# Kernel optimization log

Measured on AMD Instinct MI355X. Metric: run time of the kernel, lower is better.

The kernel has to match this reference:

```python
import jax, jax.numpy as jnp
import numpy as np

DIM = 512
NUM_GROUPS = 32
EPS = 1e-6
INV_SQRT2 = 0.7071067811865476


def group_norm(x, gamma, beta):
    # x: [b, c, h, w]; GroupNorm with NUM_GROUPS groups, per-channel affine
    b, c, h, w = x.shape
    xg = x.reshape(b, NUM_GROUPS, c // NUM_GROUPS, h, w)
    mu = xg.mean(axis=(2, 3, 4), keepdims=True)
    var = xg.var(axis=(2, 3, 4), keepdims=True)
    xn = ((xg - mu) * jax.lax.rsqrt(var + EPS)).reshape(b, c, h, w)
    return xn * gamma[None, :, None, None] + beta[None, :, None, None]


def conv1x1(x, w, b):
    # 1x1 conv == per-pixel GEMM over channels. w: [out_c, in_c], b: [out_c]
    return jnp.einsum('oc,bchw->bohw', w, x) + b[None, :, None, None]


def setup_inputs() -> dict:
    key = jax.random.key(0)
    ks = jax.random.split(key, 6)
    b, c, h, w = 4, DIM, 64, 64
    q = jax.random.normal(ks[0], (b, c, h, w), dtype=jnp.float32)
    init = lambda k: jax.random.normal(k, (DIM, DIM), dtype=jnp.float32) * 0.02
    return {
        'q': q,
        'gamma': jnp.ones((DIM,), jnp.float32),
        'beta': jnp.zeros((DIM,), jnp.float32),
        'wq': init(ks[1]), 'bq': jnp.zeros((DIM,), jnp.float32),
        'wk': init(ks[2]), 'bk': jnp.zeros((DIM,), jnp.float32),
        'wv': init(ks[3]), 'bv': jnp.zeros((DIM,), jnp.float32),
        'wo': init(ks[4]), 'bo': jnp.zeros((DIM,), jnp.float32),
    }


def reference(q, gamma, beta, wq, bq, wk, bk, wv, bv, wo, bo):
    q_in = q
    x = group_norm(q, gamma, beta)  # self-attention path: v is None -> v = normed q
    qp = conv1x1(x, wq, bq)
    kp = conv1x1(x, wk, bk)
    vp = conv1x1(x, wv, bv)
    b, c, h, w = qp.shape
    qf = qp.reshape(b, c, h * w)
    kf = kp.reshape(b, c, h * w)
    vf = vp.reshape(b, c, h * w)
    # scores[b, i, j] = sum_c k[b,c,i] * q[b,c,j]; softmax over i (key axis, dim=-2)
    scores = jnp.einsum('bci,bcj->bij', kf, qf) * (c ** -0.5)
    attn = jax.nn.softmax(scores, axis=-2)
    out = jnp.einsum('bci,bij->bcj', vf, attn).reshape(b, c, h, w)
    out = conv1x1(out, wo, bo)
    return (out + q_in) * INV_SQRT2
```

## Files before the change

kernel.cpp:

```cpp
#include <hip/hip_runtime.h>

typedef __bf16 bf16;
typedef __bf16 bf16x4 __attribute__((ext_vector_type(4)));
typedef __bf16 bf16x8 __attribute__((ext_vector_type(8)));
typedef float floatx4 __attribute__((ext_vector_type(4)));
typedef float floatx16 __attribute__((ext_vector_type(16)));

#define SCALE_QK 0.044194173824159216f
#define INV_SQRT2F 0.7071067811865476f
#define TEN  8388608L
#define SBAT 2097152L

typedef const __attribute__((address_space(1))) void GV;
typedef __attribute__((address_space(3))) void SV;

__global__ __launch_bounds__(256) void detect_k(
    const unsigned* __restrict__ q, int* __restrict__ flag)
{
    __shared__ int cnt;
    if (threadIdx.x == 0) cnt = 0;
    __syncthreads();
    int c = 0;
    for (int i = threadIdx.x; i < 4096; i += 256) {
        unsigned e = (q[i] >> 7) & 0xFFu;
        c += (e >= 100u && e <= 140u) ? 1 : 0;
    }
    atomicAdd(&cnt, c);
    __syncthreads();
    if (threadIdx.x == 0) *flag = (cnt < 3000) ? 1 : 0;
}

__global__ __launch_bounds__(256) void convw_k(
    const void* w0, const void* w1, const void* w2, const void* w3,
    bf16* __restrict__ dst, const int* __restrict__ flag)
{
    const void* srcs[4] = {w0, w1, w2, w3};
    const void* s = srcs[blockIdx.y];
    bf16* d = dst + (size_t)blockIdx.y * 262144;
    const int i = (blockIdx.x * 256 + threadIdx.x) * 8;
    bf16x8 v;
    if (*flag) {
        const float* f = (const float*)s;
        #pragma unroll
        for (int r = 0; r < 8; ++r) v[r] = (bf16)f[i + r];
    } else {
        v = *(const bf16x8*)((const bf16*)s + i);
    }
    *(bf16x8*)(d + i) = v;
}

__global__ __launch_bounds__(256) void convp_k(
    const void* p0, const void* p1, const void* p2,
    const void* p3, const void* p4, const void* p5,
    float* __restrict__ dst, const int* __restrict__ flag)
{
    const void* srcs[6] = {p0, p1, p2, p3, p4, p5};
    const int f = *flag;
    for (int i = threadIdx.x; i < 3072; i += 256) {
        const void* s = srcs[i >> 9];
        const int off = i & 511;
        dst[i] = f ? ((const float*)s)[off] : (float)((const bf16*)s)[off];
    }
}

__global__ __launch_bounds__(256) void groupnorm_k(
    const void* __restrict__ qraw, const float* __restrict__ gamma,
    const float* __restrict__ beta, bf16* __restrict__ XN,
    const int* __restrict__ flag)
{
    const int tid = threadIdx.x;
    const int b = blockIdx.x >> 5, g = blockIdx.x & 31;
    const int f32 = *flag;
    const size_t base = ((size_t)b * 512 + (size_t)g * 16) * 4096;
    const float* sf = (const float*)qraw + base;
    const bf16*  sb = (const bf16*)qraw + base;

    float sum = 0.f, sq = 0.f;
    if (f32) {
        const floatx4* v4 = (const floatx4*)sf;
        for (int idx = tid; idx < 16384; idx += 256) {
            floatx4 v = v4[idx];
            #pragma unroll
            for (int r = 0; r < 4; ++r) { float f = v[r]; sum += f; sq += f * f; }
        }
    } else {
        const bf16x8* v8 = (const bf16x8*)sb;
        for (int idx = tid; idx < 8192; idx += 256) {
            bf16x8 v = v8[idx];
            #pragma unroll
            for (int r = 0; r < 8; ++r) { float f = (float)v[r]; sum += f; sq += f * f; }
        }
    }
    #pragma unroll
    for (int off = 32; off; off >>= 1) {
        sum += __shfl_down(sum, off);
        sq  += __shfl_down(sq, off);
    }
    __shared__ float sS[4], sQ[4];
    __shared__ float s_mean, s_rstd;
    const int wave = tid >> 6, lane = tid & 63;
    if (lane == 0) { sS[wave] = sum; sQ[wave] = sq; }
    __syncthreads();
    if (tid == 0) {
        float ts = sS[0] + sS[1] + sS[2] + sS[3];
        float tq = sQ[0] + sQ[1] + sQ[2] + sQ[3];
        float mean = ts * (1.0f / 65536.0f);
        float var  = tq * (1.0f / 65536.0f) - mean * mean;
        s_mean = mean;
        s_rstd = rsqrtf(fmaxf(var, 0.f) + 1e-6f);
    }
    __syncthreads();
    const float mean = s_mean, rstd = s_rstd;

    float ga[16], be[16];
    #pragma unroll
    for (int c = 0; c < 16; ++c) {
        ga[c] = gamma[g * 16 + c] * rstd;
        be[c] = beta[g * 16 + c] - mean * ga[c];
    }
    bf16* dst = XN + (size_t)b * SBAT + (size_t)g * 16;
    for (int p0 = 0; p0 < 4096; p0 += 256) {
        const int p = p0 + tid;
        bf16x8 o0, o1;
        #pragma unroll
        for (int c = 0; c < 8; ++c) {
            float v = f32 ? sf[(size_t)c * 4096 + p] : (float)sb[(size_t)c * 4096 + p];
            o0[c] = (bf16)(v * ga[c] + be[c]);
        }
        #pragma unroll
        for (int c = 0; c < 8; ++c) {
            float v = f32 ? sf[(size_t)(c + 8) * 4096 + p] : (float)sb[(size_t)(c + 8) * 4096 + p];
            o1[c] = (bf16)(v * ga[c + 8] + be[c + 8]);
        }
        bf16* dp = dst + (size_t)p * 512;
        *(bf16x8*)dp = o0;
        *(bf16x8*)(dp + 8) = o1;
    }
}

__global__ __launch_bounds__(512, 1) void fused_attn(
    const bf16* __restrict__ QKt,
    const bf16* __restrict__ V,
    bf16* __restrict__ AOt)
{
    __shared__ __align__(16) char smc[147456];

    const int tid = threadIdx.x;
    const int w = tid >> 6, lane = tid & 63;
    const int fr = lane & 15, quad = lane >> 4;
    const int l5 = lane >> 5, l31 = lane & 31;

    const int ll = blockIdx.x;
    const int xcd = ll & 7, rr = ll >> 3;
    const int b = xcd >> 1;
    const int j0 = ((xcd & 1) * 32 + rr) * 64;

    const bf16* Qb = QKt + (size_t)b * 4194304;
    const bf16* Kb = Qb + 512;
    const bf16* Vb = V + (size_t)b * SBAT;

    const int lcK = ((tid & 15) ^ ((tid >> 4) & 15)) << 3;
    const int rowK = tid >> 4;
    auto stageK = [&](int key0, int kd0, int buf) {
        char* d = smc + buf * 32768;
        const bf16* s0 = Kb + (size_t)(key0 + rowK) * 1024 + kd0 + lcK;
        #pragma unroll
        for (int rho = 0; rho < 4; ++rho)
            __builtin_amdgcn_global_load_lds((GV*)(s0 + (size_t)rho * 32 * 1024),
                (SV*)(d + rho * 8192 + tid * 16), 16, 0, 0);
    };
    const int lcV = ((tid & 3) ^ ((tid >> 3) & 3)) << 3;
    const int rowV = tid >> 2;
    auto stageV = [&](int i0, int buf) {
        char* d = smc + 65536 + buf * 32768;
        const bf16* s0 = Vb + (size_t)rowV * 4096 + i0 + lcV;
        #pragma unroll
        for (int rho = 0; rho < 4; ++rho)
            __builtin_amdgcn_global_load_lds((GV*)(s0 + (size_t)rho * 128 * 4096),
                (SV*)(d + rho * 8192 + tid * 16), 16, 0, 0);
    };
    auto stage_sub = [&](int cc, int s) {
        if (s < 3) {
            if (cc < 32) stageK(cc * 128, (s + 1) * 128, (s + 1) & 1);
            if (cc >= 1 && cc <= 32)
                stageV((cc - 1) * 128 + (s + 1) * 32, (s + 1) & 1);
        } else {
            if (cc < 31) stageK((cc + 1) * 128, 0, 0);
            if (cc < 32) stageV(cc * 128, 0);
        }
    };

    float* lsh = (float*)(smc + 131072 + 16384);

    if (w < 4) {
        const int jb = w;
        bf16x8 qf[16];
        {
            const bf16* qsrc = Qb + (size_t)(j0 + jb * 16 + fr) * 1024 + quad * 8;
            #pragma unroll
            for (int s = 0; s < 16; ++s) qf[s] = *(const bf16x8*)(qsrc + s * 32);
        }
        const int prow = jb * 16 + fr;
        const int pxor = (prow & 15) << 4;
        char* const pbase = smc + 131072 + prow * 256;
        float l_acc = 0.f;

        stageK(0, 0, 0);

        for (int cc = 0; cc <= 32; ++cc) {
            floatx4 acc_s[8] = {};
            #pragma unroll
            for (int s = 0; s < 4; ++s) {
                asm volatile("s_waitcnt vmcnt(0)" ::: "memory");
                __builtin_amdgcn_s_barrier();
                stage_sub(cc, s);
                if (cc < 32) {
                    const char* kbuf = smc + (s & 1) * 32768;
                    __builtin_amdgcn_s_setprio(1);
                    #pragma unroll
                    for (int ksl = 0; ksl < 4; ++ksl) {
                        const char* kb0 = kbuf + fr * 256 +
                            ((((ksl << 2) | quad) ^ fr) << 4);
                        #pragma unroll
                        for (int kf = 0; kf < 8; ++kf) {
                            bf16x8 kf8 = *(const bf16x8*)(kb0 + kf * 4096);
                            acc_s[kf] = __builtin_amdgcn_mfma_f32_16x16x32_bf16(
                                kf8, qf[s * 4 + ksl], acc_s[kf], 0, 0, 0);
                        }
                    }
                    __builtin_amdgcn_s_setprio(0);
                }
            }
            __builtin_amdgcn_s_barrier();
            if (cc < 32) {
                float rs = 0.f;
                #pragma unroll
                for (int kf = 0; kf < 8; ++kf) {
                    bf16x4 pk;
                    #pragma unroll
                    for (int r = 0; r < 4; ++r) {
                        float e = __expf(fminf(acc_s[kf][r] * SCALE_QK, 30.f));
                        rs += e;
                        pk[r] = (bf16)e;
                    }
                    *(bf16x4*)(pbase + ((kf * 32 + quad * 8) ^ pxor)) = pk;
                }
                rs += __shfl_xor(rs, 16);
                rs += __shfl_xor(rs, 32);
                l_acc += rs;
                asm volatile("s_waitcnt lgkmcnt(0)" ::: "memory");
            }
            __builtin_amdgcn_s_barrier();
        }
        float* lout = (float*)smc;
        if (lane < 16) lout[jb * 16 + lane] = l_acc;
        __syncthreads();
    } else {
        const int pw = w - 4;
        floatx16 acc_o[2][4] = {};


        for (int cc = 0; cc <= 32; ++cc) {
            #pragma unroll
            for (int s = 0; s < 4; ++s) {
                asm volatile("s_waitcnt vmcnt(0)" ::: "memory");
                __builtin_amdgcn_s_barrier();
                stage_sub(cc, s);
                if (cc >= 1) {
                    const char* vb = smc + 65536 + (s & 1) * 32768;
                    const char* pb = smc + 131072;
                    __builtin_amdgcn_s_setprio(1);
                    #pragma unroll
                    for (int t = 0; t < 2; ++t) {
                        bf16x8 pa[2];
                        #pragma unroll
                        for (int jf = 0; jf < 2; ++jf) {
                            const int pr = jf * 32 + l31;
                            pa[jf] = *(const bf16x8*)(pb + pr * 256 +
                                (((s * 2 + t) * 32 + l5 * 16) ^ ((pr & 15) << 4)));
                        }
                        #pragma unroll
                        for (int nf = 0; nf < 4; ++nf) {
                            const int vc = pw * 128 + nf * 32 + l31;
                            bf16x8 vb8 = *(const bf16x8*)(vb + vc * 64 +
                                ((t * 32 + l5 * 16) ^ (((vc >> 1) & 3) << 4)));
                            acc_o[0][nf] = __builtin_amdgcn_mfma_f32_32x32x16_bf16(
                                pa[0], vb8, acc_o[0][nf], 0, 0, 0);
                            acc_o[1][nf] = __builtin_amdgcn_mfma_f32_32x32x16_bf16(
                                pa[1], vb8, acc_o[1][nf], 0, 0, 0);
                        }
                    }
                    __builtin_amdgcn_s_setprio(0);
                }
            }
            __builtin_amdgcn_s_barrier();
            __builtin_amdgcn_s_barrier();
        }
        __syncthreads();
        const float* lout = (const float*)smc;

        bf16* out = AOt + (size_t)b * SBAT + (size_t)j0 * 512;
        #pragma unroll
        for (int jf = 0; jf < 2; ++jf) {
            #pragma unroll
            for (int reg = 0; reg < 16; ++reg) {
                const int j = jf * 32 + (reg & 3) + 8 * (reg >> 2) + 4 * l5;
                const float rl = 1.0f / fmaxf(lout[j], 1e-30f);
                #pragma unroll
                for (int nf = 0; nf < 4; ++nf) {
                    const int d = pw * 128 + nf * 32 + l31;
                    out[(size_t)j * 512 + d] = (bf16)(acc_o[jf][nf][reg] * rl);
                }
            }
        }
    }
}

template <int EPI>
__global__ __launch_bounds__(256, 4) void gemm_xyt(
    const bf16* __restrict__ Xb, const bf16* __restrict__ Yb,
    void* __restrict__ Cv, int N, int K, int lda, int ldb,
    long sX, long sY, long sC,
    const float* __restrict__ bias,
    const void* __restrict__ res, long sR,
    const int* __restrict__ flag)
{
    __shared__ __align__(16) bf16 smem[17408];

    const int tid  = threadIdx.x;
    const int wave = tid >> 6;
    const int lane = tid & 63;
    const int z = blockIdx.z;

    int bx = blockIdx.x, by = blockIdx.y;
    {
        const int gx = gridDim.x, gy = gridDim.y;
        const int o = by * gx + bx;
        const int xcd = o & 7, idx = o >> 3;
        if (gx == 8) {
            bx = xcd;
            by = idx;
        } else if (gx == 32 && gy == 4) {
            bx = (xcd & 1) * 16 + (idx & 15);
            by = xcd >> 1;
        }
    }

    const bf16* X = Xb + (long)z * sX;
    const bf16* Y = Yb + (long)z * sY;
    bf16*  Cb = (bf16*)Cv  + (long)z * sC;
    float* Cf = (float*)Cv + (long)z * sC;
    const int f32o = (EPI == 4) ? *flag : 0;

    const int m0 = by * 128, n0 = bx * 128;
    const int wm = (wave >> 1) * 64, wn = (wave & 1) * 64;
    const int fr = lane & 15, quad = lane >> 4;

    const int srow = tid >> 2;
    const int scol = (tid & 3) * 8;
    const bf16* pX = X + (size_t)(m0 + srow) * lda + scol;
    const bf16* pY = Y + (size_t)(n0 + srow) * ldb + scol;
    const size_t oX = (size_t)64 * lda, oY = (size_t)64 * ldb;
    char* const sb0 = (char*)smem;
    const int ldst = tid * 16;

    auto stage = [&](int k, int pb) {
        char* d = sb0 + pb * 16384;
        const bf16* x = pX + k * 32;
        const bf16* y = pY + k * 32;
        __builtin_amdgcn_global_load_lds((GV*)x,        (SV*)(d + ldst),         16, 0, 0);
        __builtin_amdgcn_global_load_lds((GV*)(x + oX), (SV*)(d + 4096 + ldst),  16, 0, 0);
        __builtin_amdgcn_global_load_lds((GV*)y,        (SV*)(d + 8192 + ldst),  16, 0, 0);
        __builtin_amdgcn_global_load_lds((GV*)(y + oY), (SV*)(d + 12288 + ldst), 16, 0, 0);
    };

    floatx4 acc[4][4] = {};
    const int NK = K >> 5;

    stage(0, 0);
    __syncthreads();

    for (int k = 0; k < NK; ++k) {
        const int p = k & 1;
        if (k + 1 < NK) stage(k + 1, 1 - p);
        const bf16* bA = smem + p * 8192;
        const bf16* bB = bA + 4096;
        bf16x8 af[4], bfr[4];
        #pragma unroll
        for (int i = 0; i < 4; ++i) {
            af[i]  = *(const bf16x8*)&bA[(wm + i * 16 + fr) * 32 + quad * 8];
            bfr[i] = *(const bf16x8*)&bB[(wn + i * 16 + fr) * 32 + quad * 8];
        }
        #pragma unroll
        for (int i = 0; i < 4; ++i)
            #pragma unroll
            for (int j = 0; j < 4; ++j)
                acc[i][j] = __builtin_amdgcn_mfma_f32_16x16x32_bf16(
                    af[i], bfr[j], acc[i][j], 0, 0, 0);
        __syncthreads();
    }

    #pragma unroll
    for (int i = 0; i < 4; ++i) {
        const int mg = m0 + wm + i * 16 + quad * 4;
        float bmr[4];
        if (EPI == 1 || EPI == 4) {
            #pragma unroll
            for (int r = 0; r < 4; ++r) bmr[r] = bias[mg + r];
        }
        #pragma unroll
        for (int j = 0; j < 4; ++j) {
            const int ng = n0 + wn + j * 16 + fr;
            #pragma unroll
            for (int r = 0; r < 4; ++r) {
                float v = acc[i][j][r];
                if (EPI == 0) v += bias[ng];
                if (EPI == 1) v += bmr[r];
                if (EPI == 4) v += bmr[r];
                acc[i][j][r] = v;
            }
        }
    }

    if (EPI != 4) {
        bf16* ct = smem;
        #pragma unroll
        for (int i = 0; i < 4; ++i)
            #pragma unroll
            for (int j = 0; j < 4; ++j)
                #pragma unroll
                for (int r = 0; r < 4; ++r)
                    ct[(wm + i * 16 + quad * 4 + r) * 132 + wn + j * 16 + fr] =
                        (bf16)acc[i][j][r];
        __syncthreads();
        #pragma unroll
        for (int w = 0; w < 8; ++w) {
            const int idx = w * 2048 + tid * 8;
            const int row = idx >> 7, col = idx & 127;
            bf16x8 v = *(const bf16x8*)&ct[row * 132 + col];
            *(bf16x8*)&Cb[(size_t)(m0 + row) * N + n0 + col] = v;
        }
    } else if (f32o) {
        float* ct = (float*)smem;
        const float* rres = (const float*)res + (size_t)z * sR;
        #pragma unroll
        for (int h = 0; h < 2; ++h) {
            if ((wave >> 1) == h) {
                #pragma unroll
                for (int i = 0; i < 4; ++i)
                    #pragma unroll
                    for (int j = 0; j < 4; ++j)
                        #pragma unroll
                        for (int r = 0; r < 4; ++r)
                            ct[(i * 16 + quad * 4 + r) * 132 + wn + j * 16 + fr] =
                                acc[i][j][r];
            }
            __syncthreads();
            #pragma unroll
            for (int w = 0; w < 8; ++w) {
                const int idx = (w * 256 + tid) * 4;
                const int row = idx >> 7, col = idx & 127;
                const size_t o = (size_t)(m0 + h * 64 + row) * N + n0 + col;
                floatx4 v = *(const floatx4*)&ct[row * 132 + col];
                floatx4 rv = *(const floatx4*)&rres[o];
                #pragma unroll
                for (int e = 0; e < 4; ++e) v[e] = (v[e] + rv[e]) * INV_SQRT2F;
                *(floatx4*)&Cf[o] = v;
            }
            __syncthreads();
        }
    } else {
        const bf16* resb = (const bf16*)res + (size_t)z * sR;
        #pragma unroll
        for (int i = 0; i < 4; ++i) {
            const int mg = m0 + wm + i * 16 + quad * 4;
            #pragma unroll
            for (int j = 0; j < 4; ++j) {
                const int ng = n0 + wn + j * 16 + fr;
                #pragma unroll
                for (int r = 0; r < 4; ++r) {
                    const size_t o = (size_t)(mg + r) * N + ng;
                    Cb[o] = (bf16)((acc[i][j][r] + (float)resb[o]) * INV_SQRT2F);
                }
            }
        }
    }
}

extern "C" void kernel_launch(void* const* d_in, const int* in_sizes, int n_in,
                              void* d_out, int out_size, void* d_ws, size_t ws_size,
                              hipStream_t stream)
{
    const void* q     = d_in[0];
    const void* gamma = d_in[1];
    const void* beta  = d_in[2];
    const void* wq    = d_in[3];
    const void* bq    = d_in[4];
    const void* wk    = d_in[5];
    const void* bk    = d_in[6];
    const void* wv    = d_in[7];
    const void* bv    = d_in[8];
    const void* wo    = d_in[9];
    const void* bo    = d_in[10];

    char* w = (char*)d_ws;
    int*   flag = (int*)w;   w += 16;
    float* Pf   = (float*)w; w += 6 * 512 * 4;
    bf16*  Wc   = (bf16*)w;  w += 4 * 262144 * 2;
    bf16*  XN   = (bf16*)w;  w += TEN * 2;
    bf16*  QKt  = (bf16*)w;  w += (size_t)4 * 4096 * 1024 * 2;
    bf16*  V    = (bf16*)w;  w += TEN * 2;
    bf16*  AOt  = XN;

    detect_k<<<dim3(1), 256, 0, stream>>>((const unsigned*)q, flag);
    convw_k<<<dim3(128, 4), 256, 0, stream>>>(wq, wk, wv, wo, Wc, flag);
    convp_k<<<dim3(1), 256, 0, stream>>>(gamma, beta, bq, bk, bv, bo, Pf, flag);

    groupnorm_k<<<dim3(128), 256, 0, stream>>>(q, Pf, Pf + 512, XN, flag);

    gemm_xyt<0><<<dim3(8, 32, 4), 256, 0, stream>>>(XN, Wc, QKt,
        1024, 512, 512, 512, SBAT, 0, (long)4096 * 1024, Pf + 1024,
        nullptr, 0, flag);
    gemm_xyt<1><<<dim3(32, 4, 4), 256, 0, stream>>>(Wc + 2 * 262144, XN, V,
        4096, 512, 512, 512, 0, SBAT, SBAT, Pf + 2048,
        nullptr, 0, flag);

    fused_attn<<<dim3(256), 512, 0, stream>>>(QKt, V, AOt);

    gemm_xyt<4><<<dim3(32, 4, 4), 256, 0, stream>>>(Wc + 3 * 262144, AOt, d_out,
        4096, 512, 512, 512, 0, SBAT, SBAT, Pf + 2560,
        q, SBAT, flag);
}
```

Before: 453.0 us.

## Double-buffer P tile and retile QK warps to remove per-chunk barriers

The P (exp-scores) buffer in shared memory is now double-buffered by chunk parity, so the score warps write the next chunk's probabilities while the PV warps consume the previous one. This removes the two extra per-chunk barriers that serialized the softmax phase against the PV MFMAs. The QK warps are retiled to a 2x2 split (32 query rows by 64 keys each), which reuses each loaded K fragment across two query fragments and keeps partial row sums per key-half, merged at the end. It costs more LDS (160KB), more registers for the doubled Q fragments and an extra sum in the epilogue.

```diff
diff --git a/kernel.cpp b/kernel.cpp
--- a/kernel.cpp
+++ b/kernel.cpp
@@ -143,7 +143,7 @@
     const bf16* __restrict__ V,
     bf16* __restrict__ AOt)
 {
-    __shared__ __align__(16) char smc[147456];
+    __shared__ __align__(16) char smc[163840];
 
     const int tid = threadIdx.x;
     const int w = tid >> 6, lane = tid & 63;
@@ -190,25 +190,28 @@
         }
     };
 
-    float* lsh = (float*)(smc + 131072 + 16384);
+    stageK(0, 0, 0);
 
     if (w < 4) {
-        const int jb = w;
-        bf16x8 qf[16];
-        {
-            const bf16* qsrc = Qb + (size_t)(j0 + jb * 16 + fr) * 1024 + quad * 8;
-            #pragma unroll
-            for (int s = 0; s < 16; ++s) qf[s] = *(const bf16x8*)(qsrc + s * 32);
-        }
-        const int prow = jb * 16 + fr;
-        const int pxor = (prow & 15) << 4;
-        char* const pbase = smc + 131072 + prow * 256;
-        float l_acc = 0.f;
-
-        stageK(0, 0, 0);
+        const int jb = w >> 1;
+        const int kw = w & 1;
+        bf16x8 qf[2][16];
+        #pragma unroll
+        for (int jj = 0; jj < 2; ++jj) {
+            const bf16* qsrc = Qb +
+                (size_t)(j0 + jb * 32 + jj * 16 + fr) * 1024 + quad * 8;
+            #pragma unroll
+            for (int s = 0; s < 16; ++s)
+                qf[jj][s] = *(const bf16x8*)(qsrc + s * 32);
+        }
+        const int kbase = (kw * 64 + fr) * 256;
+        const int pxor = fr << 4;
+        const int prow0 = (jb * 32 + fr) * 256;
+        const int pcol0 = kw * 128;
+        float l_acc0 = 0.f, l_acc1 = 0.f;
 
         for (int cc = 0; cc <= 32; ++cc) {
-            floatx4 acc_s[8] = {};
+            floatx4 acc_s[4][2] = {};
             #pragma unroll
             for (int s = 0; s < 4; ++s) {
                 asm volatile("s_waitcnt vmcnt(0)" ::: "memory");
@@ -219,46 +222,58 @@
                     __builtin_amdgcn_s_setprio(1);
                     #pragma unroll
                     for (int ksl = 0; ksl < 4; ++ksl) {
-                        const char* kb0 = kbuf + fr * 256 +
-                            ((((ksl << 2) | quad) ^ fr) << 4);
+                        bf16x8 kfr[4];
                         #pragma unroll
-                        for (int kf = 0; kf < 8; ++kf) {
-                            bf16x8 kf8 = *(const bf16x8*)(kb0 + kf * 4096);
-                            acc_s[kf] = __builtin_amdgcn_mfma_f32_16x16x32_bf16(
-                                kf8, qf[s * 4 + ksl], acc_s[kf], 0, 0, 0);
+                        for (int kf = 0; kf < 4; ++kf)
+                            kfr[kf] = *(const bf16x8*)(kbuf + kbase + kf * 4096 +
+                                ((((ksl << 2) | quad) ^ fr) << 4));
+                        #pragma unroll
+                        for (int kf = 0; kf < 4; ++kf) {
+                            acc_s[kf][0] = __builtin_amdgcn_mfma_f32_16x16x32_bf16(
+                                kfr[kf], qf[0][s * 4 + ksl], acc_s[kf][0], 0, 0, 0);
+                            acc_s[kf][1] = __builtin_amdgcn_mfma_f32_16x16x32_bf16(
+                                kfr[kf], qf[1][s * 4 + ksl], acc_s[kf][1], 0, 0, 0);
                         }
                     }
                     __builtin_amdgcn_s_setprio(0);
+                    if (s == 3) {
+                        char* pb = smc + 131072 + (cc & 1) * 16384;
+                        float rs0 = 0.f, rs1 = 0.f;
+                        #pragma unroll
+                        for (int kf = 0; kf < 4; ++kf) {
+                            const int cb = (pcol0 + kf * 32 + quad * 8) ^ pxor;
+                            bf16x4 pk0, pk1;
+                            #pragma unroll
+                            for (int r = 0; r < 4; ++r) {
+                                float e0 = __expf(fminf(acc_s[kf][0][r] * SCALE_QK, 30.f));
+                                float e1 = __expf(fminf(acc_s[kf][1][r] * SCALE_QK, 30.f));
+                                rs0 += e0; rs1 += e1;
+                                pk0[r] = (bf16)e0; pk1[r] = (bf16)e1;
+                            }
+                            *(bf16x4*)(pb + prow0 + cb) = pk0;
+                            *(bf16x4*)(pb + prow0 + 4096 + cb) = pk1;
+                        }
+                        rs0 += __shfl_xor(rs0, 16);
+                        rs0 += __shfl_xor(rs0, 32);
+                        rs1 += __shfl_xor(rs1, 16);
+                        rs1 += __shfl_xor(rs1, 32);
+                        l_acc0 += rs0; l_acc1 += rs1;
+                        asm volatile("s_waitcnt lgkmcnt(0)" ::: "memory");
+                    }
                 }
             }
-            __builtin_amdgcn_s_barrier();
-            if (cc < 32) {
-                float rs = 0.f;
-                #pragma unroll
-                for (int kf = 0; kf < 8; ++kf) {
-                    bf16x4 pk;
-                    #pragma unroll
-                    for (int r = 0; r < 4; ++r) {
-                        float e = __expf(fminf(acc_s[kf][r] * SCALE_QK, 30.f));
-                        rs += e;
-                        pk[r] = (bf16)e;
-                    }
-                    *(bf16x4*)(pbase + ((kf * 32 + quad * 8) ^ pxor)) = pk;
-                }
-                rs += __shfl_xor(rs, 16);
-                rs += __shfl_xor(rs, 32);
-                l_acc += rs;
-                asm volatile("s_waitcnt lgkmcnt(0)" ::: "memory");
-            }
-            __builtin_amdgcn_s_barrier();
-        }
-        float* lout = (float*)smc;
-        if (lane < 16) lout[jb * 16 + lane] = l_acc;
+        }
+        __syncthreads();
+        float* lp = (float*)smc;
+        if (lane < 16) {
+            lp[kw * 64 + jb * 32 + lane] = l_acc0;
+            lp[kw * 64 + jb * 32 + 16 + lane] = l_acc1;
+        }
         __syncthreads();
     } else {
         const int pw = w - 4;
+        const int pxorR = (l31 & 15) << 4;
         floatx16 acc_o[2][4] = {};
-
 
         for (int cc = 0; cc <= 32; ++cc) {
             #pragma unroll
@@ -268,17 +283,15 @@
                 stage_sub(cc, s);
                 if (cc >= 1) {
                     const char* vb = smc + 65536 + (s & 1) * 32768;
-                    const char* pb = smc + 131072;
+                    const char* pb = smc + 131072 + ((cc - 1) & 1) * 16384;
                     __builtin_amdgcn_s_setprio(1);
                     #pragma unroll
                     for (int t = 0; t < 2; ++t) {
                         bf16x8 pa[2];
                         #pragma unroll
-                        for (int jf = 0; jf < 2; ++jf) {
-                            const int pr = jf * 32 + l31;
-                            pa[jf] = *(const bf16x8*)(pb + pr * 256 +
-                                (((s * 2 + t) * 32 + l5 * 16) ^ ((pr & 15) << 4)));
-                        }
+                        for (int jf = 0; jf < 2; ++jf)
+                            pa[jf] = *(const bf16x8*)(pb + (jf * 32 + l31) * 256 +
+                                (((s * 2 + t) * 32 + l5 * 16) ^ pxorR));
                         #pragma unroll
                         for (int nf = 0; nf < 4; ++nf) {
                             const int vc = pw * 128 + nf * 32 + l31;
@@ -293,11 +306,10 @@
                     __builtin_amdgcn_s_setprio(0);
                 }
             }
-            __builtin_amdgcn_s_barrier();
-            __builtin_amdgcn_s_barrier();
         }
         __syncthreads();
-        const float* lout = (const float*)smc;
+        __syncthreads();
+        const float* lp = (const float*)smc;
 
         bf16* out = AOt + (size_t)b * SBAT + (size_t)j0 * 512;
         #pragma unroll
@@ -305,7 +317,7 @@
             #pragma unroll
             for (int reg = 0; reg < 16; ++reg) {
                 const int j = jf * 32 + (reg & 3) + 8 * (reg >> 2) + 4 * l5;
-                const float rl = 1.0f / fmaxf(lout[j], 1e-30f);
+                const float rl = 1.0f / fmaxf(lp[j] + lp[64 + j], 1e-30f);
                 #pragma unroll
                 for (int nf = 0; nf < 4; ++nf) {
                     const int d = pw * 128 + nf * 32 + l31;
```

Result: no change. 444.2 us (-1.9%).
